# Optimization experiments

Measured on AMD Instinct MI355X. Metric: run time of the kernel, lower is better.

The kernel has to match this reference:

```python
import jax, jax.numpy as jnp
import numpy as np

D_MODEL = 1024
NHEAD = 16
D_HEAD = D_MODEL // NHEAD
D_FF = 4096
B, S = 2, 2048
EPS = 1e-5


def _linear_params(key, d_in, d_out):
    kw, kb = jax.random.split(key)
    bound = 1.0 / np.sqrt(d_in)
    W = jax.random.uniform(kw, (d_out, d_in), jnp.float32, -bound, bound)
    b = jax.random.uniform(kb, (d_out,), jnp.float32, -bound, bound)
    return W, b


def setup_inputs() -> dict:
    key = jax.random.key(0)
    ks = jax.random.split(key, 8)
    x = jax.random.normal(ks[0], (B, S, D_MODEL), jnp.float32)
    Wq, bq = _linear_params(ks[1], D_MODEL, D_MODEL)
    Wk, bk = _linear_params(ks[2], D_MODEL, D_MODEL)
    Wv, bv = _linear_params(ks[3], D_MODEL, D_MODEL)
    Wo, bo = _linear_params(ks[4], D_MODEL, D_MODEL)
    W1, b1 = _linear_params(ks[5], D_MODEL, D_FF)
    W2, b2 = _linear_params(ks[6], D_FF, D_MODEL)
    g1 = jnp.ones((D_MODEL,), jnp.float32); be1 = jnp.zeros((D_MODEL,), jnp.float32)
    g2 = jnp.ones((D_MODEL,), jnp.float32); be2 = jnp.zeros((D_MODEL,), jnp.float32)
    return dict(x=x, Wq=Wq, bq=bq, Wk=Wk, bk=bk, Wv=Wv, bv=bv, Wo=Wo, bo=bo,
                W1=W1, b1=b1, W2=W2, b2=b2, g1=g1, be1=be1, g2=g2, be2=be2)


def _layernorm(x, g, b):
    mu = jnp.mean(x, axis=-1, keepdims=True)
    var = jnp.mean(jnp.square(x - mu), axis=-1, keepdims=True)
    return (x - mu) * jax.lax.rsqrt(var + EPS) * g + b


def reference(x, Wq, bq, Wk, bk, Wv, bv, Wo, bo, W1, b1, W2, b2, g1, be1, g2, be2):
    b_, s_, _ = x.shape
    # QKV projections (nn.Linear: x @ W.T + b)
    q = x @ Wq.T + bq
    k = x @ Wk.T + bk
    v = x @ Wv.T + bv
    # split heads -> [b, h, s, d_head]
    qh = q.reshape(b_, s_, NHEAD, D_HEAD).transpose(0, 2, 1, 3)
    kh = k.reshape(b_, s_, NHEAD, D_HEAD).transpose(0, 2, 1, 3)
    vh = v.reshape(b_, s_, NHEAD, D_HEAD).transpose(0, 2, 1, 3)
    scores = jnp.einsum('bhqd,bhkd->bhqk', qh, kh) / jnp.sqrt(jnp.float32(D_HEAD))
    attn_w = jax.nn.softmax(scores, axis=-1)
    attn_out = jnp.einsum('bhqk,bhkd->bhqd', attn_w, vh)
    attn_concat = attn_out.transpose(0, 2, 1, 3).reshape(b_, s_, D_MODEL)
    attn_proj = attn_concat @ Wo.T + bo
    # residual + LN1
    h = _layernorm(x + attn_proj, g1, be1)
    # FFN
    ffn = jax.nn.relu(h @ W1.T + b1) @ W2.T + b2
    # residual + LN2
    return _layernorm(h + ffn, g2, be2)
```

## Files before the change

kernel.cpp:

```cpp
#include <hip/hip_runtime.h>
#include <hip/hip_bf16.h>

#define D_MODEL 1024
#define NHEAD 16
#define D_HEAD 64
#define D_FF 4096
#define BATCH 2
#define SEQ 2048
#define M_TOK (BATCH * SEQ)
#define EPS 1e-5f
#define QKV_N 3072

using bf16 = __hip_bfloat16;
typedef __attribute__((ext_vector_type(8))) short short8;
typedef __attribute__((ext_vector_type(4))) short short4v;
typedef __attribute__((ext_vector_type(4))) float float4v;
typedef __attribute__((ext_vector_type(16))) float float16v;

__device__ __forceinline__ float b2f(unsigned short u) {
    union { unsigned int i; float f; } v; v.i = ((unsigned int)u) << 16; return v.f;
}
__device__ __forceinline__ unsigned short f2b(float f) {
    union { float f; unsigned int u; } v; v.f = f;
    unsigned int r = v.u + 0x7FFFu + ((v.u >> 16) & 1u);
    return (unsigned short)(r >> 16);
}
__device__ __forceinline__ float loadAt(const void* p, size_t i, int f32) {
    if (f32) return ((const float*)p)[i];
    return b2f(((const unsigned short*)p)[i]);
}
__device__ __forceinline__ void async16(const void* g, void* lds) {
    __builtin_amdgcn_global_load_lds(
        (const __attribute__((address_space(1))) unsigned int*)g,
        (__attribute__((address_space(3))) unsigned int*)lds, 16, 0, 0);
}

__global__ void detect_kernel(const unsigned short* __restrict__ x, int* __restrict__ flag) {
    __shared__ int cnt;
    if (threadIdx.x == 0) cnt = 0;
    __syncthreads();
    int c = 0;
    for (int i = threadIdx.x; i < 8192; i += 256) {
        unsigned short u = x[i];
        int e = (u >> 7) & 0xFF;
        if (e >= 0xF0) c++;
    }
    atomicAdd(&cnt, c);
    __syncthreads();
    if (threadIdx.x == 0) { flag[0] = (cnt > 16) ? 1 : 0; flag[1] = 0; }
}

__global__ __launch_bounds__(256) void cast_bf16_kernel(
    const void* __restrict__ src, bf16* __restrict__ dst, int n,
    const int* __restrict__ flagp) {
    const int f32 = *flagp;
    int i0 = (blockIdx.x * 256 + threadIdx.x) * 8;
    if (i0 >= n) return;
    short8 v;
    if (f32) {
        const float* pf = (const float*)src + i0;
        float4v f0 = *(const float4v*)pf;
        float4v f1 = *(const float4v*)(pf + 4);
#pragma unroll
        for (int i = 0; i < 4; i++) { v[i] = (short)f2b(f0[i]); v[4 + i] = (short)f2b(f1[i]); }
    } else {
        v = *(const short8*)((const short*)src + i0);
    }
    *(short8*)((short*)dst + i0) = v;
}

__global__ __launch_bounds__(256) void cast3_bf16_kernel(
    const void* __restrict__ s0, const void* __restrict__ s1,
    const void* __restrict__ s2, bf16* __restrict__ dst,
    const int* __restrict__ flagp) {
    const int f32 = *flagp;
    int i0 = (blockIdx.x * 256 + threadIdx.x) * 8;
    const int part = i0 >> 20;
    const int off = i0 & ((1 << 20) - 1);
    const void* src = (part == 0) ? s0 : (part == 1) ? s1 : s2;
    short8 v;
    if (f32) {
        const float* pf = (const float*)src + off;
        float4v f0 = *(const float4v*)pf;
        float4v f1 = *(const float4v*)(pf + 4);
#pragma unroll
        for (int i = 0; i < 4; i++) { v[i] = (short)f2b(f0[i]); v[4 + i] = (short)f2b(f1[i]); }
    } else {
        v = *(const short8*)((const short*)src + off);
    }
    *(short8*)((short*)dst + i0) = v;
}

__global__ __launch_bounds__(256) void cast2_bf16_kernel(
    const void* __restrict__ s0, const void* __restrict__ s1,
    bf16* __restrict__ d0, bf16* __restrict__ d1,
    const int* __restrict__ flagp) {
    const int f32 = *flagp;
    int i0 = (blockIdx.x * 256 + threadIdx.x) * 8;
    const void* src; short* dst; int off;
    if (i0 < (1 << 20)) { src = s0; dst = (short*)d0; off = i0; }
    else                { src = s1; dst = (short*)d1; off = i0 - (1 << 20); }
    short8 v;
    if (f32) {
        const float* pf = (const float*)src + off;
        float4v f0 = *(const float4v*)pf;
        float4v f1 = *(const float4v*)(pf + 4);
#pragma unroll
        for (int i = 0; i < 4; i++) { v[i] = (short)f2b(f0[i]); v[4 + i] = (short)f2b(f1[i]); }
    } else {
        v = *(const short8*)((const short*)src + off);
    }
    *(short8*)(dst + off) = v;
}

__device__ __forceinline__ void stage8(const void* src, size_t off, int f32, short* dst) {
    short8 v;
    if (f32) {
        const float* pf = (const float*)src + off;
        float4v f0 = *(const float4v*)pf;
        float4v f1 = *(const float4v*)(pf + 4);
#pragma unroll
        for (int i = 0; i < 4; i++) { v[i] = (short)f2b(f0[i]); v[4 + i] = (short)f2b(f1[i]); }
    } else {
        v = *(const short8*)((const short*)src + off);
    }
    *(short8*)dst = v;
}

template <int MF, int NF, bool RELU, bool BDYN>
__global__ __launch_bounds__(256) void gemm_mfma(
    const bf16* __restrict__ A, const void* __restrict__ B,
    const void* __restrict__ bias0, const void* __restrict__ bias1,
    const void* __restrict__ bias2, int nb1, int nb2,
    bf16* __restrict__ C, int N, int K, const int* __restrict__ inFlagp) {
    constexpr int BM = 32 * MF, BN = 32 * NF;
    __shared__ short As[BM * 64];
    __shared__ short Bs[BN * 64];
    const int tid = threadIdx.x;
    const int lane = tid & 63;
    const int wv = tid >> 6;
    const int wm = wv & 1, wn = wv >> 1;
    const int quad = lane >> 4, lrow = lane & 15;
    const int rowM = blockIdx.y * BM;
    const int rowN = blockIdx.x * BN;
    const int inf = *inFlagp;

    float4v acc[MF][NF];
    const float4v zero = {0.f, 0.f, 0.f, 0.f};
#pragma unroll
    for (int i = 0; i < MF; i++)
#pragma unroll
        for (int j = 0; j < NF; j++) acc[i][j] = zero;

    const int sRow = lane >> 3;
    const int gChunk = (lane & 7) ^ sRow;

    for (int k0 = 0; k0 < K; k0 += 64) {
#pragma unroll
        for (int rd = 0; rd < MF; rd++) {
            const short* gp = (const short*)A +
                (size_t)(rowM + rd * 32 + wv * 8 + sRow) * K + k0 + gChunk * 8;
            async16(gp, &As[rd * 2048 + wv * 512]);
        }
        if (!BDYN) {
#pragma unroll
            for (int rd = 0; rd < NF; rd++) {
                const short* gp = (const short*)B +
                    (size_t)(rowN + rd * 32 + wv * 8 + sRow) * K + k0 + gChunk * 8;
                async16(gp, &Bs[rd * 2048 + wv * 512]);
            }
        } else {
            const int brow = tid >> 2;
            const int c0 = (tid & 3) * 2;
#pragma unroll
            for (int cc = 0; cc < 2; cc++) {
                int slot = c0 + cc;
                int g = slot ^ (brow & 7);
                stage8(B, (size_t)(rowN + brow) * K + k0 + g * 8, inf,
                       &Bs[brow * 64 + slot * 8]);
            }
        }
        __syncthreads();
#pragma unroll
        for (int ks = 0; ks < 2; ks++) {
            short8 a_frag[MF], b_frag[NF];
#pragma unroll
            for (int i = 0; i < MF; i++) {
                const int row = wm * MF * 16 + i * 16 + lrow;
                const int slot = (ks * 4 + quad) ^ (row & 7);
                a_frag[i] = *(const short8*)&As[row * 64 + slot * 8];
            }
#pragma unroll
            for (int j = 0; j < NF; j++) {
                const int row = wn * NF * 16 + j * 16 + lrow;
                const int slot = (ks * 4 + quad) ^ (row & 7);
                b_frag[j] = *(const short8*)&Bs[row * 64 + slot * 8];
            }
#pragma unroll
            for (int i = 0; i < MF; i++)
#pragma unroll
                for (int j = 0; j < NF; j++)
                    acc[i][j] = __builtin_amdgcn_mfma_f32_16x16x32_bf16(
                        a_frag[i], b_frag[j], acc[i][j], 0, 0, 0);
        }
        __syncthreads();
    }

    const int mB = rowM + wm * MF * 16, nB = rowN + wn * NF * 16;
    unsigned short* Cu = (unsigned short*)C;
#pragma unroll
    for (int j = 0; j < NF; j++) {
        const int col = nB + j * 16 + lrow;
        float bv;
        if (col < nb1)      bv = loadAt(bias0, col, inf);
        else if (col < nb2) bv = loadAt(bias1, col - nb1, inf);
        else                bv = loadAt(bias2, col - nb2, inf);
#pragma unroll
        for (int i = 0; i < MF; i++) {
#pragma unroll
            for (int r = 0; r < 4; r++) {
                const int rowg = mB + i * 16 + quad * 4 + r;
                float vv = acc[i][j][r] + bv;
                if (RELU) vv = fmaxf(vv, 0.0f);
                Cu[(size_t)rowg * N + col] = f2b(vv);
            }
        }
    }
}

#define FSTRIDE 66
__global__ __launch_bounds__(128) void flash_attn_kernel(
    const bf16* __restrict__ Qb, const bf16* __restrict__ Kb,
    const bf16* __restrict__ Vb, bf16* __restrict__ O) {
    const int bid = blockIdx.x;
    const int qt = bid & 31;
    const int h  = (bid >> 5) & 15;
    const int b  = bid >> 9;
    const int q0 = qt * 64;
    const int tid = threadIdx.x;
    const int lane = tid & 63;
    const int wv = tid >> 6;
    const int half = lane >> 5;
    const int l31 = lane & 31;

    __shared__ short Ps[64 * FSTRIDE];
    __shared__ short Ks[64 * 64];
    __shared__ short Vt[64 * FSTRIDE];

    const size_t headOff = (size_t)h * D_HEAD;
    const float SCF = 0.18033688f;

    {
        int r = tid >> 1, c0 = (tid & 1) * 32;
        const short* src = (const short*)Qb + (size_t)(b * SEQ + q0 + r) * QKV_N + headOff + c0;
#pragma unroll
        for (int ch = 0; ch < 4; ch++) {
            short8 v = *(const short8*)(src + ch * 8);
            short8 o;
#pragma unroll
            for (int e = 0; e < 8; e++)
                o[e] = (short)f2b(b2f((unsigned short)v[e]) * SCF);
            *(short8*)&Ps[r * FSTRIDE + c0 + ch * 8] = o;
        }
    }
    __syncthreads();
    short8 a_q[4];
#pragma unroll
    for (int ks = 0; ks < 4; ks++)
        a_q[ks] = *(const short8*)&Ps[(wv * 32 + l31) * FSTRIDE + ks * 16 + half * 8];

    float16v o_acc[2];
    float lsum[16];
#pragma unroll
    for (int i = 0; i < 16; i++) { o_acc[0][i] = 0.f; o_acc[1][i] = 0.f; lsum[i] = 0.f; }

    const int sRow = lane >> 3;
    const int gChunk = (lane & 7) ^ sRow;

    for (int j0 = 0; j0 < SEQ; j0 += 64) {
        __syncthreads();
#pragma unroll
        for (int rd = 0; rd < 4; rd++) {
            const short* gp = (const short*)Kb +
                (size_t)(b * SEQ + j0 + rd * 16 + wv * 8 + sRow) * QKV_N + headOff + gChunk * 8;
            async16(gp, &Ks[(rd * 16 + wv * 8) * 64]);
        }
        {
            int jp = (tid & 31) * 2, d0 = (tid >> 5) * 16;
            const short* s0 = (const short*)Vb + (size_t)(b * SEQ + j0 + jp) * QKV_N + headOff + d0;
            const short* s1 = s0 + QKV_N;
            short8 v0a = *(const short8*)s0;
            short8 v0b = *(const short8*)(s0 + 8);
            short8 v1a = *(const short8*)s1;
            short8 v1b = *(const short8*)(s1 + 8);
#pragma unroll
            for (int e = 0; e < 8; e++) {
                unsigned int wa = (unsigned int)(unsigned short)v0a[e] |
                                  ((unsigned int)(unsigned short)v1a[e] << 16);
                *(unsigned int*)&Vt[(d0 + e) * FSTRIDE + jp] = wa;
                unsigned int wb = (unsigned int)(unsigned short)v0b[e] |
                                  ((unsigned int)(unsigned short)v1b[e] << 16);
                *(unsigned int*)&Vt[(d0 + 8 + e) * FSTRIDE + jp] = wb;
            }
        }
        __syncthreads();

        float16v s_acc[2];
#pragma unroll
        for (int i = 0; i < 16; i++) { s_acc[0][i] = 0.f; s_acc[1][i] = 0.f; }
#pragma unroll
        for (int ks = 0; ks < 4; ks++)
#pragma unroll
            for (int jb = 0; jb < 2; jb++) {
                const int row = jb * 32 + l31;
                const int slot = (ks * 2 + half) ^ (l31 & 7);
                short8 bfr = *(const short8*)&Ks[row * 64 + slot * 8];
                s_acc[jb] = __builtin_amdgcn_mfma_f32_32x32x16_bf16(a_q[ks], bfr, s_acc[jb], 0, 0, 0);
            }

#pragma unroll
        for (int jb = 0; jb < 2; jb++)
#pragma unroll
            for (int reg = 0; reg < 16; reg++) {
                float pv = exp2f(s_acc[jb][reg]);
                lsum[reg] += pv;
                union { float f; unsigned int u; } uu; uu.f = pv;
                const int rowC = (reg & 3) + 8 * (reg >> 2) + 4 * half;
                Ps[(wv * 32 + rowC) * FSTRIDE + jb * 32 + l31] = (short)(uu.u >> 16);
            }

#pragma unroll
        for (int ks = 0; ks < 4; ks++) {
            short8 pa = *(const short8*)&Ps[(wv * 32 + l31) * FSTRIDE + ks * 16 + half * 8];
#pragma unroll
            for (int db = 0; db < 2; db++) {
                short8 vb = *(const short8*)&Vt[(db * 32 + l31) * FSTRIDE + ks * 16 + half * 8];
                o_acc[db] = __builtin_amdgcn_mfma_f32_32x32x16_bf16(pa, vb, o_acc[db], 0, 0, 0);
            }
        }
    }

    float invl[16];
#pragma unroll
    for (int reg = 0; reg < 16; reg++) {
        float t = lsum[reg];
        t += __shfl_xor(t, 1);
        t += __shfl_xor(t, 2);
        t += __shfl_xor(t, 4);
        t += __shfl_xor(t, 8);
        t += __shfl_xor(t, 16);
        invl[reg] = 1.0f / t;
    }
    unsigned short* Ou = (unsigned short*)O;
#pragma unroll
    for (int db = 0; db < 2; db++)
#pragma unroll
        for (int reg = 0; reg < 16; reg++) {
            const int rowC = (reg & 3) + 8 * (reg >> 2) + 4 * half;
            const int rowg = b * SEQ + q0 + wv * 32 + rowC;
            Ou[(size_t)rowg * D_MODEL + headOff + db * 32 + l31] =
                f2b(o_acc[db][reg] * invl[reg]);
        }
}

template <bool OUT_F32>
__global__ __launch_bounds__(256) void add_ln_kernel(
    const void* __restrict__ X, const bf16* __restrict__ R,
    const void* __restrict__ g, const void* __restrict__ be,
    void* __restrict__ Y,
    const int* __restrict__ xFlagp, const int* __restrict__ wFlagp) {
    const int xf = *xFlagp;
    const int wf = *wFlagp;
    const int row = blockIdx.x;
    const size_t base = (size_t)row * D_MODEL;
    const int tid = threadIdx.x;
    const int i0 = tid * 4;
    __shared__ float red[256];
    float v[4];
    if (xf) {
        float4v xv = *(const float4v*)((const float*)X + base + i0);
        short4v rv = *(const short4v*)((const short*)R + base + i0);
#pragma unroll
        for (int i = 0; i < 4; i++) v[i] = xv[i] + b2f((unsigned short)rv[i]);
    } else {
        short4v xv = *(const short4v*)((const short*)X + base + i0);
        short4v rv = *(const short4v*)((const short*)R + base + i0);
#pragma unroll
        for (int i = 0; i < 4; i++) v[i] = b2f((unsigned short)xv[i]) + b2f((unsigned short)rv[i]);
    }
    float s = v[0] + v[1] + v[2] + v[3];
    red[tid] = s; __syncthreads();
    for (int s2 = 128; s2 > 0; s2 >>= 1) {
        if (tid < s2) red[tid] += red[tid + s2];
        __syncthreads();
    }
    float mu = red[0] * (1.0f / D_MODEL);
    __syncthreads();
    float s2v = 0.f;
#pragma unroll
    for (int i = 0; i < 4; i++) { float dd = v[i] - mu; s2v += dd * dd; }
    red[tid] = s2v; __syncthreads();
    for (int s2 = 128; s2 > 0; s2 >>= 1) {
        if (tid < s2) red[tid] += red[tid + s2];
        __syncthreads();
    }
    float rstd = rsqrtf(red[0] * (1.0f / D_MODEL) + EPS);
    float gv[4], bv[4];
    if (wf) {
        float4v gg = *(const float4v*)((const float*)g + i0);
        float4v bb = *(const float4v*)((const float*)be + i0);
#pragma unroll
        for (int i = 0; i < 4; i++) { gv[i] = gg[i]; bv[i] = bb[i]; }
    } else {
        short4v gg = *(const short4v*)((const short*)g + i0);
        short4v bb = *(const short4v*)((const short*)be + i0);
#pragma unroll
        for (int i = 0; i < 4; i++) { gv[i] = b2f((unsigned short)gg[i]); bv[i] = b2f((unsigned short)bb[i]); }
    }
    if (OUT_F32) {
        float4v o;
#pragma unroll
        for (int i = 0; i < 4; i++) o[i] = (v[i] - mu) * rstd * gv[i] + bv[i];
        *(float4v*)((float*)Y + base + i0) = o;
    } else {
        short4v o;
#pragma unroll
        for (int i = 0; i < 4; i++) o[i] = (short)f2b((v[i] - mu) * rstd * gv[i] + bv[i]);
        *(short4v*)((short*)Y + base + i0) = o;
    }
}

extern "C" void kernel_launch(void* const* d_in, const int* in_sizes, int n_in,
                              void* d_out, int out_size, void* d_ws, size_t ws_size,
                              hipStream_t stream) {
    const void* x  = d_in[0];
    const void* Wq = d_in[1];  const void* bq = d_in[2];
    const void* Wk = d_in[3];  const void* bk = d_in[4];
    const void* Wv = d_in[5];  const void* bv = d_in[6];
    const void* Wo = d_in[7];  const void* bo = d_in[8];
    const void* W1 = d_in[9];  const void* b1 = d_in[10];
    const void* W2 = d_in[11]; const void* b2 = d_in[12];
    const void* g1 = d_in[13]; const void* be1 = d_in[14];
    const void* g2 = d_in[15]; const void* be2 = d_in[16];

    char* ws = (char*)d_ws;
    const size_t MB = 1024 * 1024;
    bf16* xb     = (bf16*)(ws + 0 * MB);
    bf16* wqkvb  = (bf16*)(ws + 8 * MB);
    bf16* wob    = (bf16*)(ws + 14 * MB);
    bf16* qkv    = (bf16*)(ws + 16 * MB);
    bf16* concat = (bf16*)(ws + 40 * MB);
    bf16* w1b    = (bf16*)(ws + 0 * MB);
    bf16* proj   = (bf16*)(ws + 16 * MB);
    bf16* hb     = (bf16*)(ws + 8 * MB);
    bf16* ffn1   = (bf16*)(ws + 16 * MB);
    bf16* ffn2   = (bf16*)(ws + 0 * MB);
    const bool castW2 = (ws_size >= 56 * MB + 8);
    bf16* w2b    = (bf16*)(ws + 48 * MB);
    int*  flag   = (int*)(ws + (castW2 ? 56 * MB : 48 * MB));

    const int* fIn = flag;
    const int* fBf = flag + 1;

    dim3 blk(256);

    detect_kernel<<<dim3(1), blk, 0, stream>>>((const unsigned short*)x, flag);
    cast_bf16_kernel<<<dim3((M_TOK * D_MODEL / 8 + 255) / 256), blk, 0, stream>>>(x, xb, M_TOK * D_MODEL, fIn);
    cast3_bf16_kernel<<<dim3(3 * D_MODEL * D_MODEL / 8 / 256), blk, 0, stream>>>(Wq, Wk, Wv, wqkvb, fIn);
    if (castW2)
        cast_bf16_kernel<<<dim3((D_FF * D_MODEL / 8 + 255) / 256), blk, 0, stream>>>(W2, w2b, D_FF * D_MODEL, fIn);
    gemm_mfma<4, 4, false, false><<<dim3(QKV_N / 128, M_TOK / 128), blk, 0, stream>>>(
        xb, wqkvb, bq, bk, bv, 1024, 2048, qkv, QKV_N, D_MODEL, fIn);
    cast2_bf16_kernel<<<dim3(5 * D_MODEL * D_MODEL / 8 / 256), blk, 0, stream>>>(Wo, W1, wob, w1b, fIn);
    flash_attn_kernel<<<dim3(BATCH * NHEAD * (SEQ / 64)), dim3(128), 0, stream>>>(
        qkv, qkv + D_MODEL, qkv + 2 * D_MODEL, concat);
    gemm_mfma<2, 2, false, false><<<dim3(D_MODEL / 64, M_TOK / 64), blk, 0, stream>>>(
        concat, wob, bo, bo, bo, D_MODEL, D_MODEL, proj, D_MODEL, D_MODEL, fIn);
    add_ln_kernel<false><<<dim3(M_TOK), blk, 0, stream>>>(x, proj, g1, be1, hb, fIn, fIn);
    gemm_mfma<4, 4, true, false><<<dim3(D_FF / 128, M_TOK / 128), blk, 0, stream>>>(
        hb, w1b, b1, b1, b1, D_FF, D_FF, ffn1, D_FF, D_MODEL, fIn);
    if (castW2)
        gemm_mfma<2, 2, false, false><<<dim3(D_MODEL / 64, M_TOK / 64), blk, 0, stream>>>(
            ffn1, w2b, b2, b2, b2, D_MODEL, D_MODEL, ffn2, D_MODEL, D_FF, fIn);
    else
        gemm_mfma<2, 2, false, true><<<dim3(D_MODEL / 64, M_TOK / 64), blk, 0, stream>>>(
            ffn1, W2, b2, b2, b2, D_MODEL, D_MODEL, ffn2, D_MODEL, D_FF, fIn);
    add_ln_kernel<true><<<dim3(M_TOK), blk, 0, stream>>>(hb, ffn2, g2, be2, d_out, fBf, fIn);
}
```

Before: 393.6 us.

## Split attention KV tile across four waves with cross-wave reduction

```diff
diff --git a/kernel.cpp b/kernel.cpp
--- a/kernel.cpp
+++ b/kernel.cpp
@@ -228,8 +228,7 @@
     }
 }
 
-#define FSTRIDE 66
-__global__ __launch_bounds__(128) void flash_attn_kernel(
+__global__ __launch_bounds__(256) void flash_attn_kernel(
     const bf16* __restrict__ Qb, const bf16* __restrict__ Kb,
     const bf16* __restrict__ Vb, bf16* __restrict__ O) {
     const int bid = blockIdx.x;
@@ -240,34 +239,39 @@
     const int tid = threadIdx.x;
     const int lane = tid & 63;
     const int wv = tid >> 6;
+    const int qh = wv & 1;
+    const int jh = wv >> 1;
     const int half = lane >> 5;
     const int l31 = lane & 31;
 
-    __shared__ short Ps[64 * FSTRIDE];
-    __shared__ short Ks[64 * 64];
-    __shared__ short Vt[64 * FSTRIDE];
+    __shared__ __align__(16) char smem[26624];
+    short* Ab  = (short*)smem;
+    short* Ksm = (short*)(smem + 9216);
+    short* Vt  = (short*)(smem + 17408);
 
     const size_t headOff = (size_t)h * D_HEAD;
     const float SCF = 0.18033688f;
 
     {
-        int r = tid >> 1, c0 = (tid & 1) * 32;
+        int r = tid >> 2, c0 = (tid & 3) * 16;
         const short* src = (const short*)Qb + (size_t)(b * SEQ + q0 + r) * QKV_N + headOff + c0;
 #pragma unroll
-        for (int ch = 0; ch < 4; ch++) {
+        for (int ch = 0; ch < 2; ch++) {
             short8 v = *(const short8*)(src + ch * 8);
             short8 o;
 #pragma unroll
             for (int e = 0; e < 8; e++)
                 o[e] = (short)f2b(b2f((unsigned short)v[e]) * SCF);
-            *(short8*)&Ps[r * FSTRIDE + c0 + ch * 8] = o;
+            *(short8*)&Ab[r * 66 + c0 + ch * 8] = o;
         }
     }
     __syncthreads();
     short8 a_q[4];
 #pragma unroll
     for (int ks = 0; ks < 4; ks++)
-        a_q[ks] = *(const short8*)&Ps[(wv * 32 + l31) * FSTRIDE + ks * 16 + half * 8];
+        a_q[ks] = *(const short8*)&Ab[(qh * 32 + l31) * 66 + ks * 16 + half * 8];
+
+    short* Pw = &Ab[wv * 1152];
 
     float16v o_acc[2];
     float lsum[16];
@@ -280,67 +284,58 @@
     for (int j0 = 0; j0 < SEQ; j0 += 64) {
         __syncthreads();
 #pragma unroll
-        for (int rd = 0; rd < 4; rd++) {
+        for (int rd = 0; rd < 2; rd++) {
             const short* gp = (const short*)Kb +
-                (size_t)(b * SEQ + j0 + rd * 16 + wv * 8 + sRow) * QKV_N + headOff + gChunk * 8;
-            async16(gp, &Ks[(rd * 16 + wv * 8) * 64]);
+                (size_t)(b * SEQ + j0 + rd * 32 + wv * 8 + sRow) * QKV_N + headOff + gChunk * 8;
+            async16(gp, &Ksm[(rd * 32 + wv * 8) * 64]);
         }
         {
-            int jp = (tid & 31) * 2, d0 = (tid >> 5) * 16;
+            int jp = (tid & 31) * 2, d0 = (tid >> 5) * 8;
             const short* s0 = (const short*)Vb + (size_t)(b * SEQ + j0 + jp) * QKV_N + headOff + d0;
             const short* s1 = s0 + QKV_N;
-            short8 v0a = *(const short8*)s0;
-            short8 v0b = *(const short8*)(s0 + 8);
-            short8 v1a = *(const short8*)s1;
-            short8 v1b = *(const short8*)(s1 + 8);
+            short8 v0 = *(const short8*)s0;
+            short8 v1 = *(const short8*)s1;
 #pragma unroll
             for (int e = 0; e < 8; e++) {
-                unsigned int wa = (unsigned int)(unsigned short)v0a[e] |
-                                  ((unsigned int)(unsigned short)v1a[e] << 16);
-                *(unsigned int*)&Vt[(d0 + e) * FSTRIDE + jp] = wa;
-                unsigned int wb = (unsigned int)(unsigned short)v0b[e] |
-                                  ((unsigned int)(unsigned short)v1b[e] << 16);
-                *(unsigned int*)&Vt[(d0 + 8 + e) * FSTRIDE + jp] = wb;
+                unsigned int wa = (unsigned int)(unsigned short)v0[e] |
+                                  ((unsigned int)(unsigned short)v1[e] << 16);
+                *(unsigned int*)&Vt[(d0 + e) * 66 + jp] = wa;
             }
         }
         __syncthreads();
 
-        float16v s_acc[2];
-#pragma unroll
-        for (int i = 0; i < 16; i++) { s_acc[0][i] = 0.f; s_acc[1][i] = 0.f; }
-#pragma unroll
-        for (int ks = 0; ks < 4; ks++)
-#pragma unroll
-            for (int jb = 0; jb < 2; jb++) {
-                const int row = jb * 32 + l31;
-                const int slot = (ks * 2 + half) ^ (l31 & 7);
-                short8 bfr = *(const short8*)&Ks[row * 64 + slot * 8];
-                s_acc[jb] = __builtin_amdgcn_mfma_f32_32x32x16_bf16(a_q[ks], bfr, s_acc[jb], 0, 0, 0);
-            }
-
-#pragma unroll
-        for (int jb = 0; jb < 2; jb++)
-#pragma unroll
-            for (int reg = 0; reg < 16; reg++) {
-                float pv = exp2f(s_acc[jb][reg]);
-                lsum[reg] += pv;
-                union { float f; unsigned int u; } uu; uu.f = pv;
-                const int rowC = (reg & 3) + 8 * (reg >> 2) + 4 * half;
-                Ps[(wv * 32 + rowC) * FSTRIDE + jb * 32 + l31] = (short)(uu.u >> 16);
-            }
-
+        float16v s_acc;
+#pragma unroll
+        for (int i = 0; i < 16; i++) s_acc[i] = 0.f;
 #pragma unroll
         for (int ks = 0; ks < 4; ks++) {
-            short8 pa = *(const short8*)&Ps[(wv * 32 + l31) * FSTRIDE + ks * 16 + half * 8];
+            const int row = jh * 32 + l31;
+            const int slot = (ks * 2 + half) ^ (row & 7);
+            short8 bfr = *(const short8*)&Ksm[row * 64 + slot * 8];
+            s_acc = __builtin_amdgcn_mfma_f32_32x32x16_bf16(a_q[ks], bfr, s_acc, 0, 0, 0);
+        }
+
+#pragma unroll
+        for (int reg = 0; reg < 16; reg++) {
+            float pv = exp2f(s_acc[reg]);
+            lsum[reg] += pv;
+            union { float f; unsigned int u; } uu; uu.f = pv;
+            const int rowC = (reg & 3) + 8 * (reg >> 2) + 4 * half;
+            Pw[rowC * 34 + l31] = (short)(uu.u >> 16);
+        }
+
+#pragma unroll
+        for (int ks = 0; ks < 2; ks++) {
+            short8 pa = *(const short8*)&Pw[l31 * 34 + ks * 16 + half * 8];
 #pragma unroll
             for (int db = 0; db < 2; db++) {
-                short8 vb = *(const short8*)&Vt[(db * 32 + l31) * FSTRIDE + ks * 16 + half * 8];
-                o_acc[db] = __builtin_amdgcn_mfma_f32_32x32x16_bf16(pa, vb, o_acc[db], 0, 0, 0);
-            }
-        }
-    }
-
-    float invl[16];
+                short8 vbf = *(const short8*)&Vt[(db * 32 + l31) * 66 + jh * 32 + ks * 16 + half * 8];
+                o_acc[db] = __builtin_amdgcn_mfma_f32_32x32x16_bf16(pa, vbf, o_acc[db], 0, 0, 0);
+            }
+        }
+    }
+
+    float lred[16];
 #pragma unroll
     for (int reg = 0; reg < 16; reg++) {
         float t = lsum[reg];
@@ -349,18 +344,43 @@
         t += __shfl_xor(t, 4);
         t += __shfl_xor(t, 8);
         t += __shfl_xor(t, 16);
-        invl[reg] = 1.0f / t;
-    }
-    unsigned short* Ou = (unsigned short*)O;
-#pragma unroll
-    for (int db = 0; db < 2; db++)
+        lred[reg] = t;
+    }
+
+    __syncthreads();
+    float* Red  = (float*)smem;
+    float* RedL = (float*)(smem + 16384);
+    if (jh == 1) {
 #pragma unroll
         for (int reg = 0; reg < 16; reg++) {
             const int rowC = (reg & 3) + 8 * (reg >> 2) + 4 * half;
-            const int rowg = b * SEQ + q0 + wv * 32 + rowC;
-            Ou[(size_t)rowg * D_MODEL + headOff + db * 32 + l31] =
-                f2b(o_acc[db][reg] * invl[reg]);
-        }
+#pragma unroll
+            for (int db = 0; db < 2; db++)
+                Red[(qh * 32 + rowC) * 64 + db * 32 + l31] = o_acc[db][reg];
+        }
+        if (l31 == 0) {
+#pragma unroll
+            for (int reg = 0; reg < 16; reg++) {
+                const int rowC = (reg & 3) + 8 * (reg >> 2) + 4 * half;
+                RedL[qh * 32 + rowC] = lred[reg];
+            }
+        }
+    }
+    __syncthreads();
+    if (jh == 0) {
+        unsigned short* Ou = (unsigned short*)O;
+#pragma unroll
+        for (int reg = 0; reg < 16; reg++) {
+            const int rowC = (reg & 3) + 8 * (reg >> 2) + 4 * half;
+            const float li = 1.0f / (lred[reg] + RedL[qh * 32 + rowC]);
+            const int rowg = b * SEQ + q0 + qh * 32 + rowC;
+#pragma unroll
+            for (int db = 0; db < 2; db++) {
+                float ov = o_acc[db][reg] + Red[(qh * 32 + rowC) * 64 + db * 32 + l31];
+                Ou[(size_t)rowg * D_MODEL + headOff + db * 32 + l31] = f2b(ov * li);
+            }
+        }
+    }
 }
 
 template <bool OUT_F32>
@@ -472,7 +492,7 @@
     gemm_mfma<4, 4, false, false><<<dim3(QKV_N / 128, M_TOK / 128), blk, 0, stream>>>(
         xb, wqkvb, bq, bk, bv, 1024, 2048, qkv, QKV_N, D_MODEL, fIn);
     cast2_bf16_kernel<<<dim3(5 * D_MODEL * D_MODEL / 8 / 256), blk, 0, stream>>>(Wo, W1, wob, w1b, fIn);
-    flash_attn_kernel<<<dim3(BATCH * NHEAD * (SEQ / 64)), dim3(128), 0, stream>>>(
+    flash_attn_kernel<<<dim3(BATCH * NHEAD * (SEQ / 64)), dim3(256), 0, stream>>>(
         qkv, qkv + D_MODEL, qkv + 2 * D_MODEL, concat);
     gemm_mfma<2, 2, false, false><<<dim3(D_MODEL / 64, M_TOK / 64), blk, 0, stream>>>(
         concat, wob, bo, bo, bo, D_MODEL, D_MODEL, proj, D_MODEL, D_MODEL, fIn);
```

New measurement: 474.6 us. +20.6%, slower.

## Double-buffer K/V tiles and use 128-query blocks in flash attention

Applied to the files above, without the earlier changes.

```diff
diff --git a/kernel.cpp b/kernel.cpp
--- a/kernel.cpp
+++ b/kernel.cpp
@@ -229,23 +229,23 @@
 }
 
 #define FSTRIDE 66
-__global__ __launch_bounds__(128) void flash_attn_kernel(
+__global__ __launch_bounds__(256) void flash_attn_kernel(
     const bf16* __restrict__ Qb, const bf16* __restrict__ Kb,
     const bf16* __restrict__ Vb, bf16* __restrict__ O) {
     const int bid = blockIdx.x;
-    const int qt = bid & 31;
-    const int h  = (bid >> 5) & 15;
-    const int b  = bid >> 9;
-    const int q0 = qt * 64;
+    const int qt = bid & 15;
+    const int h  = (bid >> 4) & 15;
+    const int b  = bid >> 8;
+    const int q0 = qt * 128;
     const int tid = threadIdx.x;
     const int lane = tid & 63;
     const int wv = tid >> 6;
     const int half = lane >> 5;
     const int l31 = lane & 31;
 
-    __shared__ short Ps[64 * FSTRIDE];
-    __shared__ short Ks[64 * 64];
-    __shared__ short Vt[64 * FSTRIDE];
+    __shared__ short Ab[128 * FSTRIDE];
+    __shared__ short Ks[2][64 * 64];
+    __shared__ short Vt[2][64 * FSTRIDE];
 
     const size_t headOff = (size_t)h * D_HEAD;
     const float SCF = 0.18033688f;
@@ -260,50 +260,61 @@
 #pragma unroll
             for (int e = 0; e < 8; e++)
                 o[e] = (short)f2b(b2f((unsigned short)v[e]) * SCF);
-            *(short8*)&Ps[r * FSTRIDE + c0 + ch * 8] = o;
-        }
+            *(short8*)&Ab[r * FSTRIDE + c0 + ch * 8] = o;
+        }
+    }
+
+    const int sRow = lane >> 3;
+    const int gChunk = (lane & 7) ^ sRow;
+    const int vjp = (tid & 31) * 2;
+    const int vd0 = (tid >> 5) * 8;
+
+#pragma unroll
+    for (int rd = 0; rd < 2; rd++) {
+        const short* gp = (const short*)Kb +
+            (size_t)(b * SEQ + rd * 32 + wv * 8 + sRow) * QKV_N + headOff + gChunk * 8;
+        async16(gp, &Ks[0][(rd * 32 + wv * 8) * 64]);
+    }
+    short8 v0, v1;
+    {
+        const short* s0 = (const short*)Vb + (size_t)(b * SEQ + vjp) * QKV_N + headOff + vd0;
+        v0 = *(const short8*)s0;
+        v1 = *(const short8*)(s0 + QKV_N);
     }
     __syncthreads();
+
     short8 a_q[4];
 #pragma unroll
     for (int ks = 0; ks < 4; ks++)
-        a_q[ks] = *(const short8*)&Ps[(wv * 32 + l31) * FSTRIDE + ks * 16 + half * 8];
+        a_q[ks] = *(const short8*)&Ab[(wv * 32 + l31) * FSTRIDE + ks * 16 + half * 8];
+
+#pragma unroll
+    for (int e = 0; e < 8; e++) {
+        unsigned int wa = (unsigned int)(unsigned short)v0[e] |
+                          ((unsigned int)(unsigned short)v1[e] << 16);
+        *(unsigned int*)&Vt[0][(vd0 + e) * FSTRIDE + vjp] = wa;
+    }
+    __syncthreads();
 
     float16v o_acc[2];
     float lsum[16];
 #pragma unroll
     for (int i = 0; i < 16; i++) { o_acc[0][i] = 0.f; o_acc[1][i] = 0.f; lsum[i] = 0.f; }
 
-    const int sRow = lane >> 3;
-    const int gChunk = (lane & 7) ^ sRow;
-
-    for (int j0 = 0; j0 < SEQ; j0 += 64) {
-        __syncthreads();
-#pragma unroll
-        for (int rd = 0; rd < 4; rd++) {
+    int cb = 0;
+    for (int t = 0; t < SEQ / 64; t++) {
+        const int jn = (t < SEQ / 64 - 1) ? (t + 1) * 64 : t * 64;
+#pragma unroll
+        for (int rd = 0; rd < 2; rd++) {
             const short* gp = (const short*)Kb +
-                (size_t)(b * SEQ + j0 + rd * 16 + wv * 8 + sRow) * QKV_N + headOff + gChunk * 8;
-            async16(gp, &Ks[(rd * 16 + wv * 8) * 64]);
+                (size_t)(b * SEQ + jn + rd * 32 + wv * 8 + sRow) * QKV_N + headOff + gChunk * 8;
+            async16(gp, &Ks[cb ^ 1][(rd * 32 + wv * 8) * 64]);
         }
         {
-            int jp = (tid & 31) * 2, d0 = (tid >> 5) * 16;
-            const short* s0 = (const short*)Vb + (size_t)(b * SEQ + j0 + jp) * QKV_N + headOff + d0;
-            const short* s1 = s0 + QKV_N;
-            short8 v0a = *(const short8*)s0;
-            short8 v0b = *(const short8*)(s0 + 8);
-            short8 v1a = *(const short8*)s1;
-            short8 v1b = *(const short8*)(s1 + 8);
-#pragma unroll
-            for (int e = 0; e < 8; e++) {
-                unsigned int wa = (unsigned int)(unsigned short)v0a[e] |
-                                  ((unsigned int)(unsigned short)v1a[e] << 16);
-                *(unsigned int*)&Vt[(d0 + e) * FSTRIDE + jp] = wa;
-                unsigned int wb = (unsigned int)(unsigned short)v0b[e] |
-                                  ((unsigned int)(unsigned short)v1b[e] << 16);
-                *(unsigned int*)&Vt[(d0 + 8 + e) * FSTRIDE + jp] = wb;
-            }
-        }
-        __syncthreads();
+            const short* s0 = (const short*)Vb + (size_t)(b * SEQ + jn + vjp) * QKV_N + headOff + vd0;
+            v0 = *(const short8*)s0;
+            v1 = *(const short8*)(s0 + QKV_N);
+        }
 
         float16v s_acc[2];
 #pragma unroll
@@ -314,7 +325,7 @@
             for (int jb = 0; jb < 2; jb++) {
                 const int row = jb * 32 + l31;
                 const int slot = (ks * 2 + half) ^ (l31 & 7);
-                short8 bfr = *(const short8*)&Ks[row * 64 + slot * 8];
+                short8 bfr = *(const short8*)&Ks[cb][row * 64 + slot * 8];
                 s_acc[jb] = __builtin_amdgcn_mfma_f32_32x32x16_bf16(a_q[ks], bfr, s_acc[jb], 0, 0, 0);
             }
 
@@ -326,18 +337,27 @@
                 lsum[reg] += pv;
                 union { float f; unsigned int u; } uu; uu.f = pv;
                 const int rowC = (reg & 3) + 8 * (reg >> 2) + 4 * half;
-                Ps[(wv * 32 + rowC) * FSTRIDE + jb * 32 + l31] = (short)(uu.u >> 16);
+                Ab[(wv * 32 + rowC) * FSTRIDE + jb * 32 + l31] = (short)(uu.u >> 16);
             }
 
 #pragma unroll
         for (int ks = 0; ks < 4; ks++) {
-            short8 pa = *(const short8*)&Ps[(wv * 32 + l31) * FSTRIDE + ks * 16 + half * 8];
+            short8 pa = *(const short8*)&Ab[(wv * 32 + l31) * FSTRIDE + ks * 16 + half * 8];
 #pragma unroll
             for (int db = 0; db < 2; db++) {
-                short8 vb = *(const short8*)&Vt[(db * 32 + l31) * FSTRIDE + ks * 16 + half * 8];
-                o_acc[db] = __builtin_amdgcn_mfma_f32_32x32x16_bf16(pa, vb, o_acc[db], 0, 0, 0);
-            }
-        }
+                short8 vbf = *(const short8*)&Vt[cb][(db * 32 + l31) * FSTRIDE + ks * 16 + half * 8];
+                o_acc[db] = __builtin_amdgcn_mfma_f32_32x32x16_bf16(pa, vbf, o_acc[db], 0, 0, 0);
+            }
+        }
+
+#pragma unroll
+        for (int e = 0; e < 8; e++) {
+            unsigned int wa = (unsigned int)(unsigned short)v0[e] |
+                              ((unsigned int)(unsigned short)v1[e] << 16);
+            *(unsigned int*)&Vt[cb ^ 1][(vd0 + e) * FSTRIDE + vjp] = wa;
+        }
+        __syncthreads();
+        cb ^= 1;
     }
 
     float invl[16];
@@ -472,7 +492,7 @@
     gemm_mfma<4, 4, false, false><<<dim3(QKV_N / 128, M_TOK / 128), blk, 0, stream>>>(
         xb, wqkvb, bq, bk, bv, 1024, 2048, qkv, QKV_N, D_MODEL, fIn);
     cast2_bf16_kernel<<<dim3(5 * D_MODEL * D_MODEL / 8 / 256), blk, 0, stream>>>(Wo, W1, wob, w1b, fIn);
-    flash_attn_kernel<<<dim3(BATCH * NHEAD * (SEQ / 64)), dim3(128), 0, stream>>>(
+    flash_attn_kernel<<<dim3(BATCH * NHEAD * (SEQ / 128)), dim3(256), 0, stream>>>(
         qkv, qkv + D_MODEL, qkv + 2 * D_MODEL, concat);
     gemm_mfma<2, 2, false, false><<<dim3(D_MODEL / 64, M_TOK / 64), blk, 0, stream>>>(
         concat, wob, bo, bo, bo, D_MODEL, D_MODEL, proj, D_MODEL, D_MODEL, fIn);
```

Result: faster. 380.7 us (-3.3%).
